# Performance work log

Measured on AMD Instinct MI355X. Metric: run time of the kernel, lower is better.

Reference implementation:

```python
import jax, jax.numpy as jnp
import numpy as np

V, PV, D, H, NC = 100000, 50, 128, 128, 2
L, B = 512, 64


def setup_inputs() -> dict:
    key = jax.random.key(0)
    ks = jax.random.split(key, 20)
    s = 0.05
    x = jax.random.randint(ks[0], (L, B), 0, V)
    y = jax.random.randint(ks[1], (B,), 0, 2)
    p = jax.random.randint(ks[2], (L, B), 0, PV)
    # pack_padded_sequence requires descending lengths
    lengths = jnp.sort(jax.random.randint(ks[3], (B,), 1, L + 1))[::-1]
    idx = jnp.arange(L, dtype=jnp.int32)
    left_child = jnp.broadcast_to(idx - 1, (B, L))  # left-deep chain; -1 => no child
    right_child = jnp.full((B, L), -1, dtype=jnp.int32)
    return dict(
        x=x, y=y, p=p, lengths=lengths,
        left_child=left_child, right_child=right_child,
        embed=jax.random.normal(ks[4], (V, D)) * s,
        Wih_f=jax.random.normal(ks[5], (4 * H, D)) * s,
        Whh_f=jax.random.normal(ks[6], (4 * H, H)) * s,
        b_f=jnp.zeros((4 * H,)),
        Wih_b=jax.random.normal(ks[7], (4 * H, D)) * s,
        Whh_b=jax.random.normal(ks[8], (4 * H, H)) * s,
        b_b=jnp.zeros((4 * H,)),
        Wiou=jax.random.normal(ks[9], (D, 3 * H)) * s,
        Uiou=jax.random.normal(ks[10], (H, 3 * H)) * s,
        biou=jnp.zeros((3 * H,)),
        Wf=jax.random.normal(ks[11], (D, H)) * s,
        Uf=jax.random.normal(ks[12], (H, H)) * s,
        bf=jnp.zeros((H,)),
        Wout=jax.random.normal(ks[13], (NC, 2 * H)) * s,
        bout=jnp.zeros((NC,)),
        w1=jnp.ones(()),
        w2=jnp.ones(()),
    )


def _lstm_dir(emb, mask, Wih, Whh, b, reverse):
    # length-masked uni-directional LSTM (emulates packed sequence); PyTorch gate order i,f,g,o
    Bm = emb.shape[1]
    def step(carry, inp):
        h, c = carry
        xt, m = inp  # [B,D], [B,1]
        g = xt @ Wih.T + h @ Whh.T + b
        i, f, gg, o = jnp.split(g, 4, axis=-1)
        cn = jax.nn.sigmoid(f) * c + jax.nn.sigmoid(i) * jnp.tanh(gg)
        hn = jax.nn.sigmoid(o) * jnp.tanh(cn)
        return (jnp.where(m, hn, h), jnp.where(m, cn, c)), None
    init = (jnp.zeros((Bm, H), emb.dtype), jnp.zeros((Bm, H), emb.dtype))
    (hT, _cT), _ = jax.lax.scan(step, init, (emb, mask), reverse=reverse)
    return hT  # final hidden [B,H]


def _tree_lstm(emb_k, length, left, right, Wiou, Uiou, biou, Wf, Uf, bf):
    # child-sum binary tree LSTM over one sample; nodes in topological order
    x_iou = emb_k @ Wiou + biou  # [L,3H]
    x_f = emb_k @ Wf + bf        # [L,H]
    def step(carry, inp):
        h_all, c_all = carry
        j, li, ri = inp
        def child(ix):
            v = (ix >= 0).astype(emb_k.dtype)
            ixc = jnp.maximum(ix, 0)
            return h_all[ixc] * v, c_all[ixc] * v
        hl, cl = child(li)
        hr, cr = child(ri)
        iou = x_iou[j] + (hl + hr) @ Uiou
        i, o, u = jnp.split(iou, 3)
        fl = jax.nn.sigmoid(x_f[j] + hl @ Uf)
        fr = jax.nn.sigmoid(x_f[j] + hr @ Uf)
        c = jax.nn.sigmoid(i) * jnp.tanh(u) + fl * cl + fr * cr
        h = jax.nn.sigmoid(o) * jnp.tanh(c)
        return (h_all.at[j].set(h), c_all.at[j].set(c)), None
    init = (jnp.zeros((L, H), emb_k.dtype), jnp.zeros((L, H), emb_k.dtype))
    (h_all, c_all), _ = jax.lax.scan(
        step, init, (jnp.arange(L, dtype=jnp.int32), left, right))
    root = length - 1  # last valid node is the root of the chain
    return c_all[root], h_all[root]


def reference(x, y, p, lengths, left_child, right_child, embed,
              Wih_f, Whh_f, b_f, Wih_b, Whh_b, b_b,
              Wiou, Uiou, biou, Wf, Uf, bf, Wout, bout, w1, w2):
    emb = embed[x]  # [L,B,D]; dropout layers treated as identity (eval)
    mask = (jnp.arange(L)[:, None] < lengths[None, :])[:, :, None]
    sent_vec = _lstm_dir(emb, mask, Wih_f, Whh_f, b_f, False)  # hidden[0][0], [B,H]
    _hb = _lstm_dir(emb, mask, Wih_b, Whh_b, b_b, True)        # bwd dir (unused downstream)
    emb_b = jnp.transpose(emb, (1, 0, 2))  # [B,L,D]
    t_state, t_hidden = jax.vmap(
        lambda e, ln, l, r: _tree_lstm(e, ln, l, r, Wiou, Uiou, biou, Wf, Uf, bf)
    )(emb_b, lengths, left_child, right_child)  # [B,H] each
    t_hidden = w1 * t_hidden + w2 * sent_vec    # learned mix of tree root hidden & sentence vec
    tree_out = jnp.concatenate([t_state, t_hidden], axis=1)  # [B,2H]
    pred = jax.nn.sigmoid(tree_out @ Wout.T + bout)           # [B,2]
    true = jax.nn.one_hot(jnp.clip(y, 0, 1), NC, dtype=pred.dtype)
    pc = jnp.clip(pred, 1e-7, 1.0 - 1e-7)
    loss = -jnp.mean(true * jnp.log(pc) + (1.0 - true) * jnp.log(1.0 - pc))
    return loss
```

## Files before the change

kernel.cpp:

```cpp
#include <hip/hip_runtime.h>

typedef unsigned short u16;
typedef __attribute__((ext_vector_type(8))) short bf16x8;
typedef __attribute__((ext_vector_type(4))) float f32x4;

#define LSEQ 512
#define BN   64
#define DD   128
#define HH   128
#define CHUNK 64


__device__ __forceinline__ u16 f2b(float f) {
  union { float f; unsigned i; } v; v.f = f;
  unsigned i = v.i;
  return (u16)((i + 0x7fffu + ((i >> 16) & 1u)) >> 16);
}
__device__ __forceinline__ unsigned cvt_pk_bf16(float lo, float hi) {
  unsigned r;
  asm("v_cvt_pk_bf16_f32 %0, %1, %2" : "=v"(r) : "v"(lo), "v"(hi));
  return r;
}
__device__ __forceinline__ float rcpf(float x) {
  return __builtin_amdgcn_rcpf(x);
}
__device__ __forceinline__ float sigm(float x) {
  return rcpf(1.f + __expf(-x));
}
__device__ __forceinline__ float tanh_f(float x) {
  x = fminf(15.f, fmaxf(-15.f, x));
  float e = __expf(2.f * x);
  return (e - 1.f) * rcpf(e + 1.f);
}


__global__ __launch_bounds__(512, 1) void eiou_kernel(
    const int* __restrict__ x, const int* __restrict__ lengths,
    const float* __restrict__ embed,
    const float* __restrict__ Wih_f, const float* __restrict__ b_f,
    const float* __restrict__ Wiou, const float* __restrict__ biou,
    const float* __restrict__ Wf, const float* __restrict__ bfv,
    float* __restrict__ xfwd, float* __restrict__ xtree) {
  const bool tree = blockIdx.x >= BN;
  const int b = blockIdx.x & (BN - 1);
  int len = lengths[b];
  len = (len < 1) ? 1 : (len > LSEQ ? LSEQ : len);
  const int tid = threadIdx.x;
  const int w = tid >> 6, l = tid & 63, lr = l & 15, lq = l >> 4;
  const int d = w * 16 + lr;

  __shared__ __align__(16) u16 echunk[CHUNK * 128];
  __shared__ int toks[LSEQ];

  bf16x8 bfragE[4][4];
  if (!tree) {
#pragma unroll
    for (int g = 0; g < 4; g++) {
      const int n = g * 128 + w * 16 + lr;
#pragma unroll
      for (int ks = 0; ks < 4; ks++) {
        const int k0 = ks * 32 + lq * 8;
        float4 lo = *(const float4*)(Wih_f + n * 128 + k0);
        float4 hi = *(const float4*)(Wih_f + n * 128 + k0 + 4);
        bf16x8 fr;
        fr[0] = (short)f2b(lo.x); fr[1] = (short)f2b(lo.y);
        fr[2] = (short)f2b(lo.z); fr[3] = (short)f2b(lo.w);
        fr[4] = (short)f2b(hi.x); fr[5] = (short)f2b(hi.y);
        fr[6] = (short)f2b(hi.z); fr[7] = (short)f2b(hi.w);
        bfragE[g][ks] = fr;
      }
    }
  } else {
#pragma unroll
    for (int g = 0; g < 4; g++) {
      const int col = (g < 3) ? (g * 128 + w * 16 + lr) : (w * 16 + lr);
#pragma unroll
      for (int ks = 0; ks < 4; ks++) {
        const int k0 = ks * 32 + lq * 8;
        bf16x8 fe;
#pragma unroll
        for (int j = 0; j < 8; j++) {
          const int k = k0 + j;
          float ve = (g < 3) ? Wiou[k * 384 + col] : Wf[k * 128 + col];
          fe[j] = (short)f2b(ve);
        }
        bfragE[g][ks] = fe;
      }
    }
  }

  float bias0, bias1, bias2, bias3;
  if (!tree) {
    bias0 = b_f[d];        bias1 = b_f[128 + d];
    bias2 = b_f[256 + d];  bias3 = b_f[384 + d];
  } else {
    bias0 = biou[d];       bias1 = biou[128 + d];
    bias2 = biou[256 + d]; bias3 = bfv[d];
  }

  for (int i = tid; i < LSEQ; i += 512) {
    int tt = (i < len) ? i : (len - 1);
    toks[i] = x[tt * BN + b];
  }

  float* const gbase = (tree ? xtree : xfwd) + (size_t)b * (LSEQ * 512);
  const f32x4 zf = (f32x4){0.f, 0.f, 0.f, 0.f};

  for (int c0 = 0; c0 < LSEQ; c0 += CHUNK) {
    __syncthreads();
#pragma unroll
    for (int j = 0; j < 4; j++) {
      int u = tid + j * 512;
      int r = u >> 5;
      int c4 = (u & 31) * 4;
      int row = toks[c0 + r];
      float4 v = *(const float4*)(embed + (size_t)row * DD + c4);
      unsigned p01 = cvt_pk_bf16(v.x, v.y);
      unsigned p23 = cvt_pk_bf16(v.z, v.w);
      unsigned long long packed =
          (unsigned long long)p01 | ((unsigned long long)p23 << 32);
      int bo = (r * 256 + c4 * 2) ^ ((r & 7) << 4);
      *(unsigned long long*)((char*)echunk + bo) = packed;
    }
    __syncthreads();

    for (int t0 = c0; t0 < c0 + CHUNK; t0 += 16) {
      const int rb = (t0 & (CHUNK - 1)) + lr;
      bf16x8 ae[4];
#pragma unroll
      for (int ks = 0; ks < 4; ks++) {
        int bo = (rb * 256 + ks * 64 + lq * 16) ^ ((rb & 7) << 4);
        ae[ks] = *(const bf16x8*)((const char*)echunk + bo);
      }
      f32x4 EBv[4];
#pragma unroll
      for (int g = 0; g < 4; g++)
        EBv[g] = __builtin_amdgcn_mfma_f32_16x16x32_bf16(ae[0], bfragE[g][0],
                                                         zf, 0, 0, 0);
#pragma unroll
      for (int ks = 1; ks < 4; ks++)
#pragma unroll
        for (int g = 0; g < 4; g++)
          EBv[g] = __builtin_amdgcn_mfma_f32_16x16x32_bf16(
              ae[ks], bfragE[g][ks], EBv[g], 0, 0, 0);
#pragma unroll
      for (int rg = 0; rg < 4; rg++) {
        float4 wv = {EBv[0][rg] + bias0, EBv[1][rg] + bias1,
                     EBv[2][rg] + bias2, EBv[3][rg] + bias3};
        *(float4*)(gbase + ((size_t)(t0 + lq * 4 + rg) * 512 + d * 4)) = wv;
      }
    }
  }
}

__global__ __launch_bounds__(512, 1) void chains_fast(
    const int* __restrict__ lengths,
    const float* __restrict__ Whh_f,
    const float* __restrict__ Uiou, const float* __restrict__ Uf,
    const float* __restrict__ xfwd, const float* __restrict__ xtree,
    float* __restrict__ sent_vec, float* __restrict__ t_state,
    float* __restrict__ t_hidden) {
  const bool tree = blockIdx.x >= BN;
  const int b = blockIdx.x & (BN - 1);
  int len = lengths[b];
  len = (len < 1) ? 1 : (len > LSEQ ? LSEQ : len);
  const int tid = threadIdx.x;
  const int w = tid >> 6, l = tid & 63, lr = l & 15, lq = l >> 4;
  const int d = w * 16 + lr;

  __shared__ __align__(16) u16 aK[2][128];

  bf16x8 bfragH[4][4];
  if (!tree) {
#pragma unroll
    for (int g = 0; g < 4; g++) {
      const int n = g * 128 + w * 16 + lr;
#pragma unroll
      for (int ks = 0; ks < 4; ks++) {
        const int k0 = ks * 32 + lq * 8;
        float4 lo = *(const float4*)(Whh_f + n * 128 + k0);
        float4 hi = *(const float4*)(Whh_f + n * 128 + k0 + 4);
        bf16x8 fr;
        fr[0] = (short)f2b(lo.x); fr[1] = (short)f2b(lo.y);
        fr[2] = (short)f2b(lo.z); fr[3] = (short)f2b(lo.w);
        fr[4] = (short)f2b(hi.x); fr[5] = (short)f2b(hi.y);
        fr[6] = (short)f2b(hi.z); fr[7] = (short)f2b(hi.w);
        bfragH[g][ks] = fr;
      }
    }
  } else {
#pragma unroll
    for (int g = 0; g < 4; g++) {
      const int col = (g < 3) ? (g * 128 + w * 16 + lr) : (w * 16 + lr);
#pragma unroll
      for (int ks = 0; ks < 4; ks++) {
        const int k0 = ks * 32 + lq * 8;
        bf16x8 fh;
#pragma unroll
        for (int j = 0; j < 8; j++) {
          const int k = k0 + j;
          float vh = (g < 3) ? Uiou[k * 384 + col] : Uf[k * 128 + col];
          fh[j] = (short)f2b(vh);
        }
        bfragH[g][ks] = fh;
      }
    }
  }

  if (tid < HH) { aK[0][tid] = 0; aK[1][tid] = 0; }

  const char* const ak_rd = (const char*)aK + (lq << 4);
  u16* const ak_wr = &aK[0][0] + d;

  const float* const xbase =
      (tree ? xtree : xfwd) + (size_t)b * (LSEQ * 512) + (size_t)d * 4;

  const f32x4 zf = (f32x4){0.f, 0.f, 0.f, 0.f};
  float c = 0.f, h = 0.f;
  int t = 0;

  float4 ev_e = *(const float4*)(xbase + 0 * 512);
  float4 ev_o = *(const float4*)(xbase + 1 * 512);

  __syncthreads();

#define STEPF(PAR, EVREG)                                                     \
  {                                                                           \
    bf16x8 ah[4];                                                             \
    _Pragma("unroll")                                                         \
    for (int ks = 0; ks < 4; ks++)                                            \
      ah[ks] = *(const bf16x8*)(ak_rd + (PAR) * 256 + ks * 64);               \
    f32x4 accA[4], accB[4], accC[4], accD[4];                                 \
    _Pragma("unroll")                                                         \
    for (int g = 0; g < 4; g++) {                                             \
      accA[g] = __builtin_amdgcn_mfma_f32_16x16x32_bf16(ah[0], bfragH[g][0],  \
                                                        zf, 0, 0, 0);         \
      accB[g] = __builtin_amdgcn_mfma_f32_16x16x32_bf16(ah[1], bfragH[g][1],  \
                                                        zf, 0, 0, 0);         \
      accC[g] = __builtin_amdgcn_mfma_f32_16x16x32_bf16(ah[2], bfragH[g][2],  \
                                                        zf, 0, 0, 0);         \
      accD[g] = __builtin_amdgcn_mfma_f32_16x16x32_bf16(ah[3], bfragH[g][3],  \
                                                        zf, 0, 0, 0);         \
    }                                                                         \
    float g0 = (accA[0][0] + accB[0][0]) + (accC[0][0] + accD[0][0]) +        \
               (EVREG).x;                                                     \
    float g1 = (accA[1][0] + accB[1][0]) + (accC[1][0] + accD[1][0]) +        \
               (EVREG).y;                                                     \
    float g2 = (accA[2][0] + accB[2][0]) + (accC[2][0] + accD[2][0]) +        \
               (EVREG).z;                                                     \
    float g3 = (accA[3][0] + accB[3][0]) + (accC[3][0] + accD[3][0]) +        \
               (EVREG).w;                                                     \
    if (!tree) {                                                              \
      float ii = sigm(g0), ff = sigm(g1), gg = tanh_f(g2), oo = sigm(g3);     \
      c = ff * c + ii * gg;                                                   \
      h = oo * tanh_f(c);                                                     \
    } else {                                                                  \
      float ii = sigm(g0), oo = sigm(g1), uu = tanh_f(g2), fl = sigm(g3);     \
      c = ii * uu + fl * c;                                                   \
      h = oo * tanh_f(c);                                                     \
    }                                                                         \
    unsigned hp = cvt_pk_bf16(h, h);                                          \
    if (l < 16) ak_wr[((PAR) ^ 1) * 128] = (u16)hp;                           \
    (EVREG) = *(const float4*)(xbase + (size_t)(t + 2) * 512);                \
    __syncthreads();                                                          \
    t++;                                                                      \
  }

  while (t + 2 <= len) {
    STEPF(0, ev_e)
    STEPF(1, ev_o)
  }
  if (t < len) {
    STEPF(0, ev_e)
  }
#undef STEPF

  if (l < 16) {
    if (!tree) {
      sent_vec[b * HH + d] = h;
    } else {
      t_state[b * HH + d] = c;
      t_hidden[b * HH + d] = h;
    }
  }
}

__global__ __launch_bounds__(512, 1) void chains_kernel(
    const int* __restrict__ x, const int* __restrict__ lengths,
    const float* __restrict__ embed,
    const float* __restrict__ Wih_f, const float* __restrict__ Whh_f,
    const float* __restrict__ b_f,
    const float* __restrict__ Wiou, const float* __restrict__ Uiou,
    const float* __restrict__ biou,
    const float* __restrict__ Wf, const float* __restrict__ Uf,
    const float* __restrict__ bfv,
    float* __restrict__ sent_vec, float* __restrict__ t_state,
    float* __restrict__ t_hidden) {
  const bool tree = blockIdx.x >= BN;
  const int b = blockIdx.x & (BN - 1);
  int len = lengths[b];
  len = (len < 1) ? 1 : (len > LSEQ ? LSEQ : len);
  const int tid = threadIdx.x;
  const int w = tid >> 6, l = tid & 63, lr = l & 15, lq = l >> 4;
  const int d = w * 16 + lr;

  __shared__ __align__(16) u16 echunk[CHUNK * 128];
  __shared__ __align__(16) float estage[8 * 16 * 16 * 4];
  __shared__ __align__(16) u16 aK[2][128];
  __shared__ int toks[LSEQ];

  bf16x8 bfragH[4][4], bfragE[4][4];
  if (!tree) {
#pragma unroll
    for (int g = 0; g < 4; g++) {
      const int n = g * 128 + w * 16 + lr;
#pragma unroll
      for (int ks = 0; ks < 4; ks++) {
        const int k0 = ks * 32 + lq * 8;
        {
          float4 lo = *(const float4*)(Whh_f + n * 128 + k0);
          float4 hi = *(const float4*)(Whh_f + n * 128 + k0 + 4);
          bf16x8 fr;
          fr[0] = (short)f2b(lo.x); fr[1] = (short)f2b(lo.y);
          fr[2] = (short)f2b(lo.z); fr[3] = (short)f2b(lo.w);
          fr[4] = (short)f2b(hi.x); fr[5] = (short)f2b(hi.y);
          fr[6] = (short)f2b(hi.z); fr[7] = (short)f2b(hi.w);
          bfragH[g][ks] = fr;
        }
        {
          float4 lo = *(const float4*)(Wih_f + n * 128 + k0);
          float4 hi = *(const float4*)(Wih_f + n * 128 + k0 + 4);
          bf16x8 fr;
          fr[0] = (short)f2b(lo.x); fr[1] = (short)f2b(lo.y);
          fr[2] = (short)f2b(lo.z); fr[3] = (short)f2b(lo.w);
          fr[4] = (short)f2b(hi.x); fr[5] = (short)f2b(hi.y);
          fr[6] = (short)f2b(hi.z); fr[7] = (short)f2b(hi.w);
          bfragE[g][ks] = fr;
        }
      }
    }
  } else {
#pragma unroll
    for (int g = 0; g < 4; g++) {
      const int col = (g < 3) ? (g * 128 + w * 16 + lr) : (w * 16 + lr);
#pragma unroll
      for (int ks = 0; ks < 4; ks++) {
        const int k0 = ks * 32 + lq * 8;
        bf16x8 fh, fe;
#pragma unroll
        for (int j = 0; j < 8; j++) {
          const int k = k0 + j;
          float vh, ve;
          if (g < 3) { vh = Uiou[k * 384 + col]; ve = Wiou[k * 384 + col]; }
          else       { vh = Uf[k * 128 + col];   ve = Wf[k * 128 + col]; }
          fh[j] = (short)f2b(vh);
          fe[j] = (short)f2b(ve);
        }
        bfragH[g][ks] = fh;
        bfragE[g][ks] = fe;
      }
    }
  }

  float bias0, bias1, bias2, bias3;
  if (!tree) {
    bias0 = b_f[d];        bias1 = b_f[128 + d];
    bias2 = b_f[256 + d];  bias3 = b_f[384 + d];
  } else {
    bias0 = biou[d];       bias1 = biou[128 + d];
    bias2 = biou[256 + d]; bias3 = bfv[d];
  }

  for (int i = tid; i < LSEQ; i += 512) {
    int tt = (i < len) ? i : (len - 1);
    toks[i] = x[tt * BN + b];
  }
  if (tid < HH) { aK[0][tid] = 0; aK[1][tid] = 0; }

  char* const es_base = (char*)estage;
  const int erd = (w << 12) + (lr << 4);
  const int ewr = (w << 12) + (lq << 10) + (lr << 4);
  const char* const ak_rd = (const char*)aK + (lq << 4);
  u16* const ak_wr = &aK[0][0] + d;

  const f32x4 zf = (f32x4){0.f, 0.f, 0.f, 0.f};
  float c = 0.f, h = 0.f;
  int t = 0;

#define EBATCH(T0)                                                            \
  {                                                                           \
    const int rb = ((T0) & (CHUNK - 1)) + lr;                                 \
    bf16x8 ae[4];                                                             \
    _Pragma("unroll")                                                         \
    for (int ks = 0; ks < 4; ks++) {                                          \
      int bo = (rb * 256 + ks * 64 + lq * 16) ^ ((rb & 7) << 4);              \
      ae[ks] = *(const bf16x8*)((const char*)echunk + bo);                    \
    }                                                                         \
    f32x4 EBv[4];                                                             \
    _Pragma("unroll")                                                         \
    for (int g = 0; g < 4; g++)                                               \
      EBv[g] = __builtin_amdgcn_mfma_f32_16x16x32_bf16(ae[0], bfragE[g][0],   \
                                                       zf, 0, 0, 0);          \
    _Pragma("unroll")                                                         \
    for (int ks = 1; ks < 4; ks++)                                            \
      _Pragma("unroll")                                                       \
      for (int g = 0; g < 4; g++)                                             \
        EBv[g] = __builtin_amdgcn_mfma_f32_16x16x32_bf16(                     \
            ae[ks], bfragE[g][ks], EBv[g], 0, 0, 0);                          \
    _Pragma("unroll")                                                         \
    for (int rg = 0; rg < 4; rg++) {                                          \
      f32x4 wv = {EBv[0][rg] + bias0, EBv[1][rg] + bias1,                     \
                  EBv[2][rg] + bias2, EBv[3][rg] + bias3};                    \
      *(f32x4*)(es_base + ewr + rg * 256) = wv;                               \
    }                                                                         \
  }

#define STEPB(S)                                                              \
  {                                                                           \
    bf16x8 ah[4];                                                             \
    _Pragma("unroll")                                                         \
    for (int ks = 0; ks < 4; ks++)                                            \
      ah[ks] = *(const bf16x8*)(ak_rd + ((S) & 1) * 256 + ks * 64);           \
    f32x4 ev = *(const f32x4*)(es_base + erd + (S) * 256);                    \
    f32x4 accA[4], accB[4];                                                   \
    _Pragma("unroll")                                                         \
    for (int g = 0; g < 4; g++) {                                             \
      accA[g] = __builtin_amdgcn_mfma_f32_16x16x32_bf16(ah[0], bfragH[g][0],  \
                                                        zf, 0, 0, 0);         \
      accB[g] = __builtin_amdgcn_mfma_f32_16x16x32_bf16(ah[2], bfragH[g][2],  \
                                                        zf, 0, 0, 0);         \
    }                                                                         \
    _Pragma("unroll")                                                         \
    for (int g = 0; g < 4; g++) {                                             \
      accA[g] = __builtin_amdgcn_mfma_f32_16x16x32_bf16(                      \
          ah[1], bfragH[g][1], accA[g], 0, 0, 0);                             \
      accB[g] = __builtin_amdgcn_mfma_f32_16x16x32_bf16(                      \
          ah[3], bfragH[g][3], accB[g], 0, 0, 0);                             \
    }                                                                         \
    float g0 = accA[0][0] + accB[0][0] + ev[0];                               \
    float g1 = accA[1][0] + accB[1][0] + ev[1];                               \
    float g2 = accA[2][0] + accB[2][0] + ev[2];                               \
    float g3 = accA[3][0] + accB[3][0] + ev[3];                               \
    if (!tree) {                                                              \
      float ii = sigm(g0), ff = sigm(g1), gg = tanh_f(g2), oo = sigm(g3);     \
      c = ff * c + ii * gg;                                                   \
      h = oo * tanh_f(c);                                                     \
    } else {                                                                  \
      float ii = sigm(g0), oo = sigm(g1), uu = tanh_f(g2), fl = sigm(g3);     \
      c = ii * uu + fl * c;                                                   \
      h = oo * tanh_f(c);                                                     \
    }                                                                         \
    unsigned hp = cvt_pk_bf16(h, h);                                          \
    if (l < 16) ak_wr[(((S) & 1) ^ 1) * 128] = (u16)hp;                       \
    __syncthreads();                                                          \
  }

#define STEPT(S) if (tb + (S) < tend) STEPB(S)

  for (int c0 = 0; c0 < len; c0 += CHUNK) {
    __syncthreads();
#pragma unroll
    for (int j = 0; j < 4; j++) {
      int u = tid + j * 512;
      int r = u >> 5;
      int c4 = (u & 31) * 4;
      int row = toks[c0 + r];
      float4 v = *(const float4*)(embed + (size_t)row * DD + c4);
      unsigned p01 = cvt_pk_bf16(v.x, v.y);
      unsigned p23 = cvt_pk_bf16(v.z, v.w);
      unsigned long long packed =
          (unsigned long long)p01 | ((unsigned long long)p23 << 32);
      int bo = (r * 256 + c4 * 2) ^ ((r & 7) << 4);
      *(unsigned long long*)((char*)echunk + bo) = packed;
    }
    __syncthreads();

    const int tend = (c0 + CHUNK < len) ? c0 + CHUNK : len;
    while (t + 16 <= tend) {
      EBATCH(t)
      STEPB(0)  STEPB(1)  STEPB(2)  STEPB(3)
      STEPB(4)  STEPB(5)  STEPB(6)  STEPB(7)
      STEPB(8)  STEPB(9)  STEPB(10) STEPB(11)
      STEPB(12) STEPB(13) STEPB(14) STEPB(15)
      t += 16;
    }
    if (t < tend) {
      const int tb = t;
      EBATCH(tb)
      STEPT(0)  STEPT(1)  STEPT(2)  STEPT(3)
      STEPT(4)  STEPT(5)  STEPT(6)  STEPT(7)
      STEPT(8)  STEPT(9)  STEPT(10) STEPT(11)
      STEPT(12) STEPT(13) STEPT(14)
      t = tend;
    }
  }
#undef STEPT
#undef STEPB
#undef EBATCH

  if (l < 16) {
    if (!tree) {
      sent_vec[b * HH + d] = h;
    } else {
      t_state[b * HH + d] = c;
      t_hidden[b * HH + d] = h;
    }
  }
}

__global__ __launch_bounds__(128) void final_kernel(
    const int* __restrict__ y, const float* __restrict__ sent_vec,
    const float* __restrict__ t_state, const float* __restrict__ t_hidden,
    const float* __restrict__ Wout, const float* __restrict__ bout,
    const float* __restrict__ w1, const float* __restrict__ w2,
    float* __restrict__ out) {
  int tid = threadIdx.x;
  int b = tid >> 1, cls = tid & 1;
  float W1 = w1[0], W2 = w2[0];
  const float* wrow = Wout + cls * 256;
  float acc = bout[cls];
  for (int j = 0; j < HH; j++)
    acc += t_state[b * HH + j] * wrow[j];
  for (int j = 0; j < HH; j++)
    acc += (W1 * t_hidden[b * HH + j] + W2 * sent_vec[b * HH + j]) * wrow[128 + j];
  float p = 1.f / (1.f + __expf(-acc));
  p = fminf(1.f - 1e-7f, fmaxf(1e-7f, p));
  int yy = y[b]; yy = yy < 0 ? 0 : (yy > 1 ? 1 : yy);
  float term = (cls == yy) ? __logf(p) : __logf(1.f - p);
  __shared__ float red[128];
  red[tid] = term;
  __syncthreads();
  for (int s = 64; s > 0; s >>= 1) {
    if (tid < s) red[tid] += red[tid + s];
    __syncthreads();
  }
  if (tid == 0) out[0] = -red[0] / 128.f;
}

extern "C" void kernel_launch(void* const* d_in, const int* in_sizes, int n_in,
                              void* d_out, int out_size, void* d_ws, size_t ws_size,
                              hipStream_t stream) {
  (void)in_sizes; (void)n_in; (void)out_size;
  const int*   x       = (const int*)d_in[0];
  const int*   y       = (const int*)d_in[1];
  const int*   lengths = (const int*)d_in[3];
  const float* embed   = (const float*)d_in[6];
  const float* Wih_f   = (const float*)d_in[7];
  const float* Whh_f   = (const float*)d_in[8];
  const float* b_f     = (const float*)d_in[9];
  const float* Wiou    = (const float*)d_in[13];
  const float* Uiou    = (const float*)d_in[14];
  const float* biou    = (const float*)d_in[15];
  const float* Wf      = (const float*)d_in[16];
  const float* Uf      = (const float*)d_in[17];
  const float* bfv     = (const float*)d_in[18];
  const float* Wout    = (const float*)d_in[19];
  const float* bout    = (const float*)d_in[20];
  const float* w1      = (const float*)d_in[21];
  const float* w2      = (const float*)d_in[22];

  float* sent_vec = (float*)d_ws;
  float* t_state  = sent_vec + BN * HH;
  float* t_hidden = t_state + BN * HH;
  const size_t out_bytes = (size_t)BN * HH * 3 * sizeof(float);
  const size_t x4_bytes  = (size_t)BN * LSEQ * 512 * sizeof(float);
  const size_t need = out_bytes + 2 * x4_bytes + (1u << 20);

  if (ws_size >= need) {
    float* xfwd  = (float*)((char*)d_ws + out_bytes);
    float* xtree = xfwd + (size_t)BN * LSEQ * 512;
    eiou_kernel<<<128, 512, 0, stream>>>(x, lengths, embed, Wih_f, b_f,
                                         Wiou, biou, Wf, bfv, xfwd, xtree);
    chains_fast<<<128, 512, 0, stream>>>(lengths, Whh_f, Uiou, Uf,
                                         xfwd, xtree,
                                         sent_vec, t_state, t_hidden);
  } else {
    chains_kernel<<<128, 512, 0, stream>>>(x, lengths, embed,
                                           Wih_f, Whh_f, b_f,
                                           Wiou, Uiou, biou, Wf, Uf, bfv,
                                           sent_vec, t_state, t_hidden);
  }
  final_kernel<<<1, 128, 0, stream>>>(y, sent_vec, t_state, t_hidden,
                                      Wout, bout, w1, w2, (float*)d_out);
}
```

Measured before the change: 416.6 us.

## Split input-projection kernel across sequence chunks and lighten recurrent step barrier

The precompute kernel now launches one block per (batch, direction, 64-step chunk) instead of looping over all chunks in 128 blocks, and blocks whose chunk starts past the sequence length exit early. This spreads the embedding gather and input GEMM across many more CUs and skips padded timesteps. In the recurrent chain kernel, the next-step input load is issued before the MFMAs, and the full __syncthreads is replaced by an LDS-only waitcnt plus a raw s_barrier, so the global prefetch stays in flight across the barrier. The cost is that each new block reloads and converts the weight fragments, and the hand-written barrier depends on only LDS writes needing to be visible.

```diff
diff --git a/kernel.cpp b/kernel.cpp
--- a/kernel.cpp
+++ b/kernel.cpp
@@ -41,16 +41,20 @@
     const float* __restrict__ Wiou, const float* __restrict__ biou,
     const float* __restrict__ Wf, const float* __restrict__ bfv,
     float* __restrict__ xfwd, float* __restrict__ xtree) {
-  const bool tree = blockIdx.x >= BN;
-  const int b = blockIdx.x & (BN - 1);
+  const int bid = blockIdx.x;
+  const int b = bid & (BN - 1);
+  const bool tree = (bid >> 6) & 1;
+  const int c0 = (bid >> 7) * CHUNK;
   int len = lengths[b];
   len = (len < 1) ? 1 : (len > LSEQ ? LSEQ : len);
+  if (c0 >= len) return;
+
   const int tid = threadIdx.x;
   const int w = tid >> 6, l = tid & 63, lr = l & 15, lq = l >> 4;
   const int d = w * 16 + lr;
 
   __shared__ __align__(16) u16 echunk[CHUNK * 128];
-  __shared__ int toks[LSEQ];
+  __shared__ int toks_s[CHUNK];
 
   bf16x8 bfragE[4][4];
   if (!tree) {
@@ -98,57 +102,57 @@
     bias2 = biou[256 + d]; bias3 = bfv[d];
   }
 
-  for (int i = tid; i < LSEQ; i += 512) {
+  if (tid < CHUNK) {
+    int i = c0 + tid;
     int tt = (i < len) ? i : (len - 1);
-    toks[i] = x[tt * BN + b];
-  }
+    toks_s[tid] = x[tt * BN + b];
+  }
+  __syncthreads();
+
+#pragma unroll
+  for (int j = 0; j < 4; j++) {
+    int u = tid + j * 512;
+    int r = u >> 5;
+    int c4 = (u & 31) * 4;
+    int row = toks_s[r];
+    float4 v = *(const float4*)(embed + (size_t)row * DD + c4);
+    unsigned p01 = cvt_pk_bf16(v.x, v.y);
+    unsigned p23 = cvt_pk_bf16(v.z, v.w);
+    unsigned long long packed =
+        (unsigned long long)p01 | ((unsigned long long)p23 << 32);
+    int bo = (r * 256 + c4 * 2) ^ ((r & 7) << 4);
+    *(unsigned long long*)((char*)echunk + bo) = packed;
+  }
+  __syncthreads();
 
   float* const gbase = (tree ? xtree : xfwd) + (size_t)b * (LSEQ * 512);
   const f32x4 zf = (f32x4){0.f, 0.f, 0.f, 0.f};
 
-  for (int c0 = 0; c0 < LSEQ; c0 += CHUNK) {
-    __syncthreads();
-#pragma unroll
-    for (int j = 0; j < 4; j++) {
-      int u = tid + j * 512;
-      int r = u >> 5;
-      int c4 = (u & 31) * 4;
-      int row = toks[c0 + r];
-      float4 v = *(const float4*)(embed + (size_t)row * DD + c4);
-      unsigned p01 = cvt_pk_bf16(v.x, v.y);
-      unsigned p23 = cvt_pk_bf16(v.z, v.w);
-      unsigned long long packed =
-          (unsigned long long)p01 | ((unsigned long long)p23 << 32);
-      int bo = (r * 256 + c4 * 2) ^ ((r & 7) << 4);
-      *(unsigned long long*)((char*)echunk + bo) = packed;
-    }
-    __syncthreads();
-
-    for (int t0 = c0; t0 < c0 + CHUNK; t0 += 16) {
-      const int rb = (t0 & (CHUNK - 1)) + lr;
-      bf16x8 ae[4];
-#pragma unroll
-      for (int ks = 0; ks < 4; ks++) {
-        int bo = (rb * 256 + ks * 64 + lq * 16) ^ ((rb & 7) << 4);
-        ae[ks] = *(const bf16x8*)((const char*)echunk + bo);
-      }
-      f32x4 EBv[4];
+  for (int t0 = 0; t0 < CHUNK; t0 += 16) {
+    const int rb = t0 + lr;
+    bf16x8 ae[4];
+#pragma unroll
+    for (int ks = 0; ks < 4; ks++) {
+      int bo = (rb * 256 + ks * 64 + lq * 16) ^ ((rb & 7) << 4);
+      ae[ks] = *(const bf16x8*)((const char*)echunk + bo);
+    }
+    f32x4 EBv[4];
+#pragma unroll
+    for (int g = 0; g < 4; g++)
+      EBv[g] = __builtin_amdgcn_mfma_f32_16x16x32_bf16(ae[0], bfragE[g][0],
+                                                       zf, 0, 0, 0);
+#pragma unroll
+    for (int ks = 1; ks < 4; ks++)
 #pragma unroll
       for (int g = 0; g < 4; g++)
-        EBv[g] = __builtin_amdgcn_mfma_f32_16x16x32_bf16(ae[0], bfragE[g][0],
-                                                         zf, 0, 0, 0);
-#pragma unroll
-      for (int ks = 1; ks < 4; ks++)
-#pragma unroll
-        for (int g = 0; g < 4; g++)
-          EBv[g] = __builtin_amdgcn_mfma_f32_16x16x32_bf16(
-              ae[ks], bfragE[g][ks], EBv[g], 0, 0, 0);
-#pragma unroll
-      for (int rg = 0; rg < 4; rg++) {
-        float4 wv = {EBv[0][rg] + bias0, EBv[1][rg] + bias1,
-                     EBv[2][rg] + bias2, EBv[3][rg] + bias3};
-        *(float4*)(gbase + ((size_t)(t0 + lq * 4 + rg) * 512 + d * 4)) = wv;
-      }
+        EBv[g] = __builtin_amdgcn_mfma_f32_16x16x32_bf16(
+            ae[ks], bfragE[g][ks], EBv[g], 0, 0, 0);
+#pragma unroll
+    for (int rg = 0; rg < 4; rg++) {
+      float4 wv = {EBv[0][rg] + bias0, EBv[1][rg] + bias1,
+                   EBv[2][rg] + bias2, EBv[3][rg] + bias3};
+      *(float4*)(gbase +
+                 ((size_t)(c0 + t0 + lq * 4 + rg) * 512 + d * 4)) = wv;
     }
   }
 }
@@ -230,6 +234,7 @@
     _Pragma("unroll")                                                         \
     for (int ks = 0; ks < 4; ks++)                                            \
       ah[ks] = *(const bf16x8*)(ak_rd + (PAR) * 256 + ks * 64);               \
+    float4 evn = *(const float4*)(xbase + (size_t)(t + 2) * 512);             \
     f32x4 accA[4], accB[4], accC[4], accD[4];                                 \
     _Pragma("unroll")                                                         \
     for (int g = 0; g < 4; g++) {                                             \
@@ -261,8 +266,10 @@
     }                                                                         \
     unsigned hp = cvt_pk_bf16(h, h);                                          \
     if (l < 16) ak_wr[((PAR) ^ 1) * 128] = (u16)hp;                           \
-    (EVREG) = *(const float4*)(xbase + (size_t)(t + 2) * 512);                \
-    __syncthreads();                                                          \
+    (EVREG) = evn;                                                            \
+    asm volatile("s_waitcnt lgkmcnt(0)" ::: "memory");                        \
+    __builtin_amdgcn_s_barrier();                                             \
+    __builtin_amdgcn_sched_barrier(0);                                        \
     t++;                                                                      \
   }
 
@@ -569,8 +576,8 @@
   if (ws_size >= need) {
     float* xfwd  = (float*)((char*)d_ws + out_bytes);
     float* xtree = xfwd + (size_t)BN * LSEQ * 512;
-    eiou_kernel<<<128, 512, 0, stream>>>(x, lengths, embed, Wih_f, b_f,
-                                         Wiou, biou, Wf, bfv, xfwd, xtree);
+    eiou_kernel<<<1024, 512, 0, stream>>>(x, lengths, embed, Wih_f, b_f,
+                                          Wiou, biou, Wf, bfv, xfwd, xtree);
     chains_fast<<<128, 512, 0, stream>>>(lengths, Whh_f, Uiou, Uf,
                                          xfwd, xtree,
                                          sent_vec, t_state, t_hidden);
```

Measured after the change: 402.2 us. 1.04x faster.
